# Kernel tuning notes

Hardware: AMD Instinct MI355X
Metric: run time of the kernel (lower is better)

Reference implementation:

```python
import jax, jax.numpy as jnp
import numpy as np
from jax import lax

B = 8192          # batched independent VAD frames (original module is batch=1 streaming)
CUTOFF = 129      # STFT_CUTOFF
STRIDE = 128      # STFT_STRIDE
NFFT = 256        # STFT kernel length (inferred: pad 576->640, stride 128 -> 4 frames)
H = 128           # LSTM hidden size


def conv1d(x, w, b=None, stride=1, padding=0):
    # x: [B, Cin, T], w: [Cout, Cin, K]
    y = lax.conv_general_dilated(x, w, (stride,), [(padding, padding)],
                                 dimension_numbers=("NCH", "OIH", "NCH"))
    if b is not None:
        y = y + b[None, :, None]
    return y


def setup_inputs() -> dict:
    key = jax.random.key(0)
    ks = jax.random.split(key, 40)
    f32 = jnp.float32

    def rn(i, shape, scale=0.1):
        return jax.random.normal(ks[i], shape, dtype=f32) * scale

    inp = {
        "audio": jax.random.normal(ks[0], (B, 576), dtype=f32),
        "h": jnp.zeros((B, H), dtype=f32),
        "c": jnp.zeros((B, H), dtype=f32),
        # STFT basis: 129 real + 129 imag cosine/sine rows, kernel 256
        "forward_basis": rn(1, (2 * CUTOFF, 1, NFFT), 0.1),
        # encoder: 4 conv1d+relu blocks (Silero v5 layout)
        "enc_w1": rn(2, (128, 129, 3)), "enc_b1": rn(3, (128,)),
        "enc_w2": rn(4, (64, 128, 3)), "enc_b2": rn(5, (64,)),
        "enc_w3": rn(6, (64, 64, 3)),  "enc_b3": rn(7, (64,)),
        "enc_w4": rn(8, (128, 64, 3)), "enc_b4": rn(9, (128,)),
        # LSTM cell weights
        "wi": rn(10, (H, H)), "wf": rn(11, (H, H)), "wg": rn(12, (H, H)), "wo": rn(13, (H, H)),
        "ui": rn(14, (H, H)), "uf": rn(15, (H, H)), "ug": rn(16, (H, H)), "uo": rn(17, (H, H)),
        "bxi": rn(18, (H,)), "bxf": rn(19, (H,)), "bxg": rn(20, (H,)), "bxo": rn(21, (H,)),
        "bhi": rn(22, (H,)), "bhf": rn(23, (H,)), "bhg": rn(24, (H,)), "bho": rn(25, (H,)),
        # output head: conv1d 128 -> 1, kernel 1
        "conv_w": rn(26, (1, H, 1)), "conv_b": rn(27, (1,)),
    }
    return inp


def reference(audio, h, c, forward_basis,
              enc_w1, enc_b1, enc_w2, enc_b2, enc_w3, enc_b3, enc_w4, enc_b4,
              wi, wf, wg, wo, ui, uf, ug, uo,
              bxi, bxf, bxg, bxo, bhi, bhf, bhg, bho,
              conv_w, conv_b):
    # STFT via strided conv1d on reflect-padded audio
    x = jnp.pad(audio, ((0, 0), (0, 64)), mode="reflect")[:, None, :]   # [B,1,640]
    x = conv1d(x, forward_basis, stride=STRIDE)                          # [B,258,4]
    real, imag = x[:, :CUTOFF, :], x[:, CUTOFF:, :]
    mag = jnp.sqrt(real ** 2 + imag ** 2)                                # [B,129,4]

    # encoder: conv+relu stack, T: 4 -> 4 -> 2 -> 1 -> 1
    e = jax.nn.relu(conv1d(mag, enc_w1, enc_b1, stride=1, padding=1))
    e = jax.nn.relu(conv1d(e, enc_w2, enc_b2, stride=2, padding=1))
    e = jax.nn.relu(conv1d(e, enc_w3, enc_b3, stride=2, padding=1))
    e = jax.nn.relu(conv1d(e, enc_w4, enc_b4, stride=1, padding=1))
    x = e[:, :, 0]                                                       # [B,128]

    lin = lambda v, W, b: v @ W.T + b
    i_gate = jax.nn.sigmoid(lin(x, wi, bxi) + lin(h, ui, bhi))
    f_gate = jax.nn.sigmoid(lin(x, wf, bxf) + lin(h, uf, bhf))
    g_gate = jnp.tanh(lin(x, wg, bxg) + lin(h, ug, bhg))
    o_gate = jax.nn.sigmoid(lin(x, wo, bxo) + lin(h, uo, bho))
    c_out = f_gate * c + i_gate * g_gate
    h_out = o_gate * jnp.tanh(c_out)

    # output head: relu -> conv1d(128->1, k=1) -> sigmoid -> mean over T(=1)
    y = jax.nn.relu(h_out)                                               # [B,128]
    logit = y @ conv_w[0, :, 0] + conv_b[0]                              # [B]
    prob = jax.nn.sigmoid(logit)[:, None]                                # [B,1]
    return prob, h_out, c_out
```

## Files before the change

kernel.cpp:

```cpp
#include <hip/hip_runtime.h>
#include <math.h>

#define BATCH 8192
typedef unsigned short u16;
typedef unsigned int u32;
typedef __attribute__((ext_vector_type(8))) short bf16x8;
typedef __attribute__((ext_vector_type(4))) float f32x4;
typedef __attribute__((ext_vector_type(4))) unsigned short u16x4;

__device__ __forceinline__ float sigm(float v) { return 1.0f / (1.0f + __expf(-v)); }
__device__ __forceinline__ u16 f2bf(float f) {
    union { float f; u32 u; } v; v.f = f;
    u32 r = v.u + 0x7FFFu + ((v.u >> 16) & 1u);
    return (u16)(r >> 16);
}
__device__ __forceinline__ float bf2f(u16 h) {
    union { u32 u; float f; } v; v.u = ((u32)h) << 16; return v.f;
}
__device__ __forceinline__ void split_store4(float4 v, u16* hp, u16* lp) {
    u16 h0 = f2bf(v.x), h1 = f2bf(v.y), h2 = f2bf(v.z), h3 = f2bf(v.w);
    u16x4 hv = {h0, h1, h2, h3};
    u16x4 lv = {f2bf(v.x - bf2f(h0)), f2bf(v.y - bf2f(h1)),
                f2bf(v.z - bf2f(h2)), f2bf(v.w - bf2f(h3))};
    *(u16x4*)hp = hv; *(u16x4*)lp = lv;
}
__device__ __forceinline__ bf16x8 bfrag(const u16* Bf, int nt, int ch, int nch, int lane) {
    return *(const bf16x8*)(Bf + (((size_t)nt * nch + ch) * 64 + lane) * 8);
}
#define MFMA(a, b, c) __builtin_amdgcn_mfma_f32_16x16x32_bf16(a, b, c, 0, 0, 0)

#define S_FBT 69632
#define S_B1  61440
#define S_B2A 16384
#define S_B2B 24576
#define S_B3  8192
#define S_B4  8192
#define S_BL  131072
#define P_FBT 0
#define P_B1  139264
#define P_B2A 262144
#define P_B2B 294912
#define P_B3  344064
#define P_B4  360448
#define P_BL  376832
#define WEND  638976
#define N_PREP 319488

__global__ __launch_bounds__(256) void k_prep(const float* __restrict__ fb,
                                              const float* __restrict__ w1, const float* __restrict__ w2,
                                              const float* __restrict__ w3, const float* __restrict__ w4,
                                              const float* __restrict__ wi, const float* __restrict__ wf,
                                              const float* __restrict__ wg, const float* __restrict__ wo,
                                              const float* __restrict__ ui, const float* __restrict__ uf,
                                              const float* __restrict__ ug, const float* __restrict__ uo,
                                              u16* __restrict__ wsu) {
    const float* Ws[8] = {wi, wf, wg, wo, ui, uf, ug, uo};
    for (int i = blockIdx.x * 256 + threadIdx.x; i < N_PREP; i += gridDim.x * 256) {
        int r = i;
        float v; int P, S, idx;
        if (r < S_FBT) {
            int f = r >> 9, lane = (r & 511) >> 3, e = r & 7;
            int n = (f >> 3) * 16 + (lane & 15), k = (f & 7) * 32 + (lane >> 4) * 8 + e;
            int c = n >> 1, part = n & 1;
            v = (n < 258) ? fb[(size_t)(c + part * 129) * 256 + k] : 0.f;
            P = P_FBT; S = S_FBT; idx = r;
        } else if ((r -= S_FBT) < S_B1) {
            int kk = r / 20480, r2 = r - kk * 20480;
            int f = r2 >> 9, lane = (r2 & 511) >> 3, e = r2 & 7;
            int n = (f / 5) * 16 + (lane & 15), k = (f % 5) * 32 + (lane >> 4) * 8 + e;
            v = (k < 129) ? w1[(size_t)n * 387 + k * 3 + kk] : 0.f;
            P = P_B1; S = S_B1; idx = r;
        } else if ((r -= S_B1) < S_B2A) {
            int f = r >> 9, lane = (r & 511) >> 3, e = r & 7;
            int n = (f >> 3) * 16 + (lane & 15), k = (f & 7) * 32 + (lane >> 4) * 8 + e;
            v = w2[(size_t)n * 384 + (k & 127) * 3 + (k >> 7) + 1];
            P = P_B2A; S = S_B2A; idx = r;
        } else if ((r -= S_B2A) < S_B2B) {
            int f = r >> 9, lane = (r & 511) >> 3, e = r & 7;
            int n = (f / 12) * 16 + (lane & 15), k = (f % 12) * 32 + (lane >> 4) * 8 + e;
            v = w2[(size_t)n * 384 + (k & 127) * 3 + (k >> 7)];
            P = P_B2B; S = S_B2B; idx = r;
        } else if ((r -= S_B2B) < S_B3) {
            int f = r >> 9, lane = (r & 511) >> 3, e = r & 7;
            int n = (f >> 2) * 16 + (lane & 15), k = (f & 3) * 32 + (lane >> 4) * 8 + e;
            v = w3[(size_t)n * 192 + (k & 63) * 3 + (k >> 6) + 1];
            P = P_B3; S = S_B3; idx = r;
        } else if ((r -= S_B3) < S_B4) {
            int f = r >> 9, lane = (r & 511) >> 3, e = r & 7;
            int n = (f >> 1) * 16 + (lane & 15), k = (f & 1) * 32 + (lane >> 4) * 8 + e;
            v = w4[(size_t)n * 192 + k * 3 + 1];
            P = P_B4; S = S_B4; idx = r;
        } else {
            r -= S_B4;
            int f = r >> 9, lane = (r & 511) >> 3, e = r & 7;
            int n = (f >> 3) * 16 + (lane & 15), k = (f & 7) * 32 + (lane >> 4) * 8 + e;
            int g = n >> 7, j = n & 127;
            v = Ws[g + ((k >= 128) ? 4 : 0)][(size_t)j * 128 + (k & 127)];
            P = P_BL; S = S_BL; idx = r;
        }
        u16 h = f2bf(v);
        wsu[P + idx] = h;
        wsu[P + S + idx] = f2bf(v - bf2f(h));
    }
}

__global__ __launch_bounds__(512) void k_fused1(const float* __restrict__ audio,
                                                const u16* __restrict__ wsu,
                                                const float* __restrict__ b1,
                                                float* __restrict__ act) {
    __shared__ __align__(16) u16 aAh[8 * 680];
    __shared__ __align__(16) u16 aAl[8 * 680];
    __shared__ __align__(16) u16 mAh[8 * 6 * 168];
    __shared__ __align__(16) u16 mAl[8 * 6 * 168];
    const int tid = threadIdx.x;
    const int b0 = blockIdx.x << 3;
    for (int i = tid; i < 4032; i += 512) {
        ((u32*)mAh)[i] = 0u;
        ((u32*)mAl)[i] = 0u;
    }
    for (int i = tid; i < 8 * 160; i += 512) {
        int bb = i / 160, j4 = (i - bb * 160) * 4;
        const float* ap = audio + (size_t)(b0 + bb) * 576;
        float4 v;
        if (j4 < 576) v = *(const float4*)(ap + j4);
        else { v.x = ap[1150 - j4]; v.y = ap[1149 - j4]; v.z = ap[1148 - j4]; v.w = ap[1147 - j4]; }
        int phys = bb * 680 + j4 + (j4 >> 7) * 8;
        split_store4(v, aAh + phys, aAl + phys);
    }
    __syncthreads();
    const int lane = tid & 63, w = tid >> 6;
    const int m = lane & 15, quad = lane >> 4;
    const u16* fbT = wsu + P_FBT;
    const int tcnt = (w == 7) ? 3 : 2;
    f32x4 acc[2][3];
    #pragma unroll
    for (int mt = 0; mt < 2; ++mt)
        #pragma unroll
        for (int t = 0; t < 3; ++t) acc[mt][t] = (f32x4){0.f, 0.f, 0.f, 0.f};
    for (int ch = 0; ch < 8; ++ch) {
        bf16x8 ah[2], al[2];
        #pragma unroll
        for (int mt = 0; mt < 2; ++mt) {
            int Rm = mt * 16 + m;
            int phys = (Rm >> 2) * 680 + (Rm & 3) * 136 + ch * 32 + quad * 8 + ((ch >= 4) ? 8 : 0);
            ah[mt] = *(const bf16x8*)(aAh + phys);
            al[mt] = *(const bf16x8*)(aAl + phys);
        }
        #pragma unroll
        for (int tt = 0; tt < 3; ++tt) {
            if (tt < tcnt) {
                int t = w * 2 + tt;
                bf16x8 bh = bfrag(fbT, t, ch, 8, lane);
                bf16x8 bl_ = bfrag(fbT + S_FBT, t, ch, 8, lane);
                #pragma unroll
                for (int mt = 0; mt < 2; ++mt) {
                    acc[mt][tt] = MFMA(ah[mt], bh, acc[mt][tt]);
                    acc[mt][tt] = MFMA(ah[mt], bl_, acc[mt][tt]);
                    acc[mt][tt] = MFMA(al[mt], bh, acc[mt][tt]);
                }
            }
        }
    }
    #pragma unroll
    for (int tt = 0; tt < 3; ++tt) {
        if (tt < tcnt) {
            int n = (w * 2 + tt) * 16 + m;
            #pragma unroll
            for (int mt = 0; mt < 2; ++mt)
                #pragma unroll
                for (int r = 0; r < 4; ++r) {
                    float vv = acc[mt][tt][r];
                    float s = vv * vv;
                    s += __shfl_xor(s, 1);
                    if (!(n & 1)) {
                        int R = mt * 16 + quad * 4 + r;
                        int bb = R >> 2, t = R & 3, c = n >> 1;
                        float sv = sqrtf(s);
                        u16 h = f2bf(sv);
                        int phys = (bb * 6 + t + 1) * 168 + c;
                        mAh[phys] = h;
                        mAl[phys] = f2bf(sv - bf2f(h));
                    }
                }
        }
    }
    __syncthreads();
    const u16* B1h = wsu + P_B1;
    const u16* B1l = wsu + P_B1 + S_B1;
    f32x4 acc2[2];
    acc2[0] = (f32x4){0.f, 0.f, 0.f, 0.f};
    acc2[1] = (f32x4){0.f, 0.f, 0.f, 0.f};
    for (int kk = 0; kk < 3; ++kk) {
        for (int ch = 0; ch < 5; ++ch) {
            bf16x8 bh = bfrag(B1h + kk * 20480, w, ch, 5, lane);
            bf16x8 bl_ = bfrag(B1l + kk * 20480, w, ch, 5, lane);
            #pragma unroll
            for (int mt = 0; mt < 2; ++mt) {
                int Rm = mt * 16 + m;
                int phys = ((Rm >> 2) * 6 + (Rm & 3) + kk) * 168 + ch * 32 + quad * 8;
                bf16x8 ah = *(const bf16x8*)(mAh + phys);
                bf16x8 al = *(const bf16x8*)(mAl + phys);
                acc2[mt] = MFMA(ah, bh, acc2[mt]);
                acc2[mt] = MFMA(ah, bl_, acc2[mt]);
                acc2[mt] = MFMA(al, bh, acc2[mt]);
            }
        }
    }
    {
        int n = w * 16 + m;
        float bv = b1[n];
        #pragma unroll
        for (int mt = 0; mt < 2; ++mt)
            #pragma unroll
            for (int r = 0; r < 4; ++r) {
                int R = mt * 16 + quad * 4 + r;
                act[(size_t)(b0 + (R >> 2)) * 512 + (R & 3) * 128 + n] = fmaxf(acc2[mt][r] + bv, 0.f);
            }
    }
}

__global__ __launch_bounds__(512) void k_fused2(const float* __restrict__ act,
                                                const float* __restrict__ hin,
                                                const u16* __restrict__ wsu,
                                                const float* __restrict__ cin,
                                                const float* __restrict__ b2, const float* __restrict__ b3,
                                                const float* __restrict__ b4,
                                                const float* __restrict__ bxi, const float* __restrict__ bxf,
                                                const float* __restrict__ bxg, const float* __restrict__ bxo,
                                                const float* __restrict__ bhi, const float* __restrict__ bhf,
                                                const float* __restrict__ bhg, const float* __restrict__ bho,
                                                const float* __restrict__ cw, const float* __restrict__ cb,
                                                float* __restrict__ out) {
    __shared__ __align__(16) u16 eAh[16 * 520];
    __shared__ __align__(16) u16 eAl[16 * 520];
    __shared__ __align__(16) u16 s2h[16 * 136];
    __shared__ __align__(16) u16 s2l[16 * 136];
    __shared__ __align__(16) u16 s3h[16 * 72];
    __shared__ __align__(16) u16 s3l[16 * 72];
    __shared__ __align__(16) u16 xhh[16 * 264];
    __shared__ __align__(16) u16 xhl[16 * 264];
    __shared__ float pr[8][16];
    const int tid = threadIdx.x;
    const int b0 = blockIdx.x << 4;
    for (int i = tid; i < 16 * 128; i += 512) {
        int row = i >> 7, c4 = (i & 127) * 4;
        float4 v = *(const float4*)(act + (size_t)(b0 + row) * 512 + c4);
        split_store4(v, eAh + row * 520 + c4, eAl + row * 520 + c4);
    }
    for (int i = tid; i < 16 * 32; i += 512) {
        int row = i >> 5, c4 = (i & 31) * 4;
        float4 v = *(const float4*)(hin + (size_t)(b0 + row) * 128 + c4);
        split_store4(v, xhh + row * 264 + 128 + c4, xhl + row * 264 + 128 + c4);
    }
    __syncthreads();
    const int lane = tid & 63, w = tid >> 6;
    const int m = lane & 15, quad = lane >> 4;
    {
        const int isB = w >> 2, nt = w & 3;
        const int awoff = isB ? 128 : 0;
        const int nch = isB ? 12 : 8;
        const u16* Bh = wsu + (isB ? P_B2B : P_B2A);
        const u16* Bl = Bh + (isB ? S_B2B : S_B2A);
        f32x4 acc = (f32x4){0.f, 0.f, 0.f, 0.f};
        for (int ch = 0; ch < nch; ++ch) {
            int phys = m * 520 + awoff + ch * 32 + quad * 8;
            bf16x8 ah = *(const bf16x8*)(eAh + phys);
            bf16x8 al = *(const bf16x8*)(eAl + phys);
            bf16x8 bh = bfrag(Bh, nt, ch, nch, lane);
            bf16x8 bl_ = bfrag(Bl, nt, ch, nch, lane);
            acc = MFMA(ah, bh, acc);
            acc = MFMA(ah, bl_, acc);
            acc = MFMA(al, bh, acc);
        }
        const int oc = nt * 16 + m;
        const float bv = b2[oc];
        const int col = isB * 64 + oc;
        #pragma unroll
        for (int r = 0; r < 4; ++r) {
            int row = quad * 4 + r;
            float vv = fmaxf(acc[r] + bv, 0.f);
            u16 h = f2bf(vv);
            s2h[row * 136 + col] = h;
            s2l[row * 136 + col] = f2bf(vv - bf2f(h));
        }
    }
    __syncthreads();
    if (w < 4) {
        const u16* Bh = wsu + P_B3;
        const u16* Bl = Bh + S_B3;
        f32x4 acc = (f32x4){0.f, 0.f, 0.f, 0.f};
        for (int ch = 0; ch < 4; ++ch) {
            int phys = m * 136 + ch * 32 + quad * 8;
            bf16x8 ah = *(const bf16x8*)(s2h + phys);
            bf16x8 al = *(const bf16x8*)(s2l + phys);
            bf16x8 bh = bfrag(Bh, w, ch, 4, lane);
            bf16x8 bl_ = bfrag(Bl, w, ch, 4, lane);
            acc = MFMA(ah, bh, acc);
            acc = MFMA(ah, bl_, acc);
            acc = MFMA(al, bh, acc);
        }
        const int n = w * 16 + m;
        const float bv = b3[n];
        #pragma unroll
        for (int r = 0; r < 4; ++r) {
            int row = quad * 4 + r;
            float vv = fmaxf(acc[r] + bv, 0.f);
            u16 h = f2bf(vv);
            s3h[row * 72 + n] = h;
            s3l[row * 72 + n] = f2bf(vv - bf2f(h));
        }
    }
    __syncthreads();
    {
        const u16* Bh = wsu + P_B4;
        const u16* Bl = Bh + S_B4;
        f32x4 acc = (f32x4){0.f, 0.f, 0.f, 0.f};
        for (int ch = 0; ch < 2; ++ch) {
            int phys = m * 72 + ch * 32 + quad * 8;
            bf16x8 ah = *(const bf16x8*)(s3h + phys);
            bf16x8 al = *(const bf16x8*)(s3l + phys);
            bf16x8 bh = bfrag(Bh, w, ch, 2, lane);
            bf16x8 bl_ = bfrag(Bl, w, ch, 2, lane);
            acc = MFMA(ah, bh, acc);
            acc = MFMA(ah, bl_, acc);
            acc = MFMA(al, bh, acc);
        }
        const int n = w * 16 + m;
        const float bv = b4[n];
        #pragma unroll
        for (int r = 0; r < 4; ++r) {
            int row = quad * 4 + r;
            float vv = fmaxf(acc[r] + bv, 0.f);
            u16 h = f2bf(vv);
            xhh[row * 264 + n] = h;
            xhl[row * 264 + n] = f2bf(vv - bf2f(h));
        }
    }
    __syncthreads();
    {
        const u16* BLh = wsu + P_BL;
        const u16* BLl = BLh + S_BL;
        f32x4 acc[4];
        #pragma unroll
        for (int g = 0; g < 4; ++g) acc[g] = (f32x4){0.f, 0.f, 0.f, 0.f};
        for (int ch = 0; ch < 8; ++ch) {
            int phys = m * 264 + ch * 32 + quad * 8;
            bf16x8 ah = *(const bf16x8*)(xhh + phys);
            bf16x8 al = *(const bf16x8*)(xhl + phys);
            #pragma unroll
            for (int g = 0; g < 4; ++g) {
                int nt = g * 8 + w;
                bf16x8 bh = bfrag(BLh, nt, ch, 8, lane);
                bf16x8 bl_ = bfrag(BLl, nt, ch, 8, lane);
                acc[g] = MFMA(ah, bh, acc[g]);
                acc[g] = MFMA(ah, bl_, acc[g]);
                acc[g] = MFMA(al, bh, acc[g]);
            }
        }
        float partial[4];
        const int j = w * 16 + m;
        const float bi = bxi[j] + bhi[j];
        const float bff = bxf[j] + bhf[j];
        const float bgg = bxg[j] + bhg[j];
        const float boo = bxo[j] + bho[j];
        const float cwj = cw[j];
        #pragma unroll
        for (int r = 0; r < 4; ++r) {
            const int b = b0 + quad * 4 + r;
            const float ig = sigm(acc[0][r] + bi);
            const float fg = sigm(acc[1][r] + bff);
            const float gg = tanhf(acc[2][r] + bgg);
            const float og = sigm(acc[3][r] + boo);
            const float ci = cin[(size_t)b * 128 + j];
            const float co = fg * ci + ig * gg;
            const float ho = og * tanhf(co);
            out[(size_t)BATCH + (size_t)b * 128 + j] = ho;
            out[(size_t)BATCH + (size_t)BATCH * 128 + (size_t)b * 128 + j] = co;
            partial[r] = fmaxf(ho, 0.f) * cwj;
        }
        #pragma unroll
        for (int off = 1; off < 16; off <<= 1)
            #pragma unroll
            for (int r = 0; r < 4; ++r) partial[r] += __shfl_xor(partial[r], off);
        if (m == 0) {
            #pragma unroll
            for (int r = 0; r < 4; ++r) pr[w][quad * 4 + r] = partial[r];
        }
    }
    __syncthreads();
    if (tid < 16) {
        float s = cb[0];
        #pragma unroll
        for (int g = 0; g < 8; ++g) s += pr[g][tid];
        out[b0 + tid] = sigm(s);
    }
}

extern "C" void kernel_launch(void* const* d_in, const int* in_sizes, int n_in,
                              void* d_out, int out_size, void* d_ws, size_t ws_size,
                              hipStream_t stream) {
    const float* audio = (const float*)d_in[0];
    const float* hin   = (const float*)d_in[1];
    const float* cin   = (const float*)d_in[2];
    const float* fb    = (const float*)d_in[3];
    const float* w1    = (const float*)d_in[4];
    const float* b1    = (const float*)d_in[5];
    const float* w2    = (const float*)d_in[6];
    const float* b2    = (const float*)d_in[7];
    const float* w3    = (const float*)d_in[8];
    const float* b3    = (const float*)d_in[9];
    const float* w4    = (const float*)d_in[10];
    const float* b4    = (const float*)d_in[11];
    const float* wi    = (const float*)d_in[12];
    const float* wf    = (const float*)d_in[13];
    const float* wg    = (const float*)d_in[14];
    const float* wo    = (const float*)d_in[15];
    const float* ui    = (const float*)d_in[16];
    const float* uf    = (const float*)d_in[17];
    const float* ug    = (const float*)d_in[18];
    const float* uo    = (const float*)d_in[19];
    const float* bxi   = (const float*)d_in[20];
    const float* bxf   = (const float*)d_in[21];
    const float* bxg   = (const float*)d_in[22];
    const float* bxo   = (const float*)d_in[23];
    const float* bhi   = (const float*)d_in[24];
    const float* bhf   = (const float*)d_in[25];
    const float* bhg   = (const float*)d_in[26];
    const float* bho   = (const float*)d_in[27];
    const float* cw    = (const float*)d_in[28];
    const float* cb    = (const float*)d_in[29];
    float* out = (float*)d_out;

    u16* wsu = (u16*)d_ws;
    float* ACT = (float*)(wsu + WEND);

    k_prep<<<640, 256, 0, stream>>>(fb, w1, w2, w3, w4, wi, wf, wg, wo, ui, uf, ug, uo, wsu);
    k_fused1<<<BATCH / 8, 512, 0, stream>>>(audio, wsu, b1, ACT);
    k_fused2<<<BATCH / 16, 512, 0, stream>>>(ACT, hin, wsu, cin, b2, b3, b4,
                                             bxi, bxf, bxg, bxo, bhi, bhf, bhg, bho,
                                             cw, cb, out);
}
```

Before: 188.0 us.

## Double batch tile in k_fused1, alias shared buffers, pass bf16 hi/lo split

k_fused1 now processes 16 frames per block instead of 8, so each B-fragment of the STFT and conv1 weights is reused across four M-tiles. The audio and magnitude shared buffers are aliased into one union, which needs an extra barrier and a re-zero pass between the phases. The intermediate activation is written as precomputed bf16 hi/lo halves instead of fp32, so k_fused2 only copies them and no longer does the split. In exchange, register pressure rises from the larger accumulator arrays and the grid has half as many blocks.

```diff
diff --git a/kernel.cpp b/kernel.cpp
--- a/kernel.cpp
+++ b/kernel.cpp
@@ -107,24 +107,21 @@
 __global__ __launch_bounds__(512) void k_fused1(const float* __restrict__ audio,
                                                 const u16* __restrict__ wsu,
                                                 const float* __restrict__ b1,
-                                                float* __restrict__ act) {
-    __shared__ __align__(16) u16 aAh[8 * 680];
-    __shared__ __align__(16) u16 aAl[8 * 680];
-    __shared__ __align__(16) u16 mAh[8 * 6 * 168];
-    __shared__ __align__(16) u16 mAl[8 * 6 * 168];
+                                                u16* __restrict__ E1H, u16* __restrict__ E1L) {
+    __shared__ __align__(16) u16 uni[32256];
+    u16* aAh = uni;
+    u16* aAl = uni + 11520;
+    u16* mAh = uni;
+    u16* mAl = uni + 16128;
     const int tid = threadIdx.x;
-    const int b0 = blockIdx.x << 3;
-    for (int i = tid; i < 4032; i += 512) {
-        ((u32*)mAh)[i] = 0u;
-        ((u32*)mAl)[i] = 0u;
-    }
-    for (int i = tid; i < 8 * 160; i += 512) {
+    const int b0 = blockIdx.x << 4;
+    for (int i = tid; i < 16 * 160; i += 512) {
         int bb = i / 160, j4 = (i - bb * 160) * 4;
         const float* ap = audio + (size_t)(b0 + bb) * 576;
         float4 v;
         if (j4 < 576) v = *(const float4*)(ap + j4);
         else { v.x = ap[1150 - j4]; v.y = ap[1149 - j4]; v.z = ap[1148 - j4]; v.w = ap[1147 - j4]; }
-        int phys = bb * 680 + j4 + (j4 >> 7) * 8;
+        int phys = bb * 720 + j4 + (j4 >> 7) * 8;
         split_store4(v, aAh + phys, aAl + phys);
     }
     __syncthreads();
@@ -132,17 +129,17 @@
     const int m = lane & 15, quad = lane >> 4;
     const u16* fbT = wsu + P_FBT;
     const int tcnt = (w == 7) ? 3 : 2;
-    f32x4 acc[2][3];
+    f32x4 acc[4][3];
     #pragma unroll
-    for (int mt = 0; mt < 2; ++mt)
+    for (int mt = 0; mt < 4; ++mt)
         #pragma unroll
         for (int t = 0; t < 3; ++t) acc[mt][t] = (f32x4){0.f, 0.f, 0.f, 0.f};
     for (int ch = 0; ch < 8; ++ch) {
-        bf16x8 ah[2], al[2];
-        #pragma unroll
-        for (int mt = 0; mt < 2; ++mt) {
+        bf16x8 ah[4], al[4];
+        #pragma unroll
+        for (int mt = 0; mt < 4; ++mt) {
             int Rm = mt * 16 + m;
-            int phys = (Rm >> 2) * 680 + (Rm & 3) * 136 + ch * 32 + quad * 8 + ((ch >= 4) ? 8 : 0);
+            int phys = (Rm >> 2) * 720 + (Rm & 3) * 136 + ch * 32 + quad * 8 + ((ch >= 4) ? 8 : 0);
             ah[mt] = *(const bf16x8*)(aAh + phys);
             al[mt] = *(const bf16x8*)(aAl + phys);
         }
@@ -153,7 +150,7 @@
                 bf16x8 bh = bfrag(fbT, t, ch, 8, lane);
                 bf16x8 bl_ = bfrag(fbT + S_FBT, t, ch, 8, lane);
                 #pragma unroll
-                for (int mt = 0; mt < 2; ++mt) {
+                for (int mt = 0; mt < 4; ++mt) {
                     acc[mt][tt] = MFMA(ah[mt], bh, acc[mt][tt]);
                     acc[mt][tt] = MFMA(ah[mt], bl_, acc[mt][tt]);
                     acc[mt][tt] = MFMA(al[mt], bh, acc[mt][tt]);
@@ -161,12 +158,15 @@
             }
         }
     }
+    __syncthreads();
+    for (int i = tid; i < 16128; i += 512) ((u32*)uni)[i] = 0u;
+    __syncthreads();
     #pragma unroll
     for (int tt = 0; tt < 3; ++tt) {
         if (tt < tcnt) {
             int n = (w * 2 + tt) * 16 + m;
             #pragma unroll
-            for (int mt = 0; mt < 2; ++mt)
+            for (int mt = 0; mt < 4; ++mt)
                 #pragma unroll
                 for (int r = 0; r < 4; ++r) {
                     float vv = acc[mt][tt][r];
@@ -187,15 +187,15 @@
     __syncthreads();
     const u16* B1h = wsu + P_B1;
     const u16* B1l = wsu + P_B1 + S_B1;
-    f32x4 acc2[2];
-    acc2[0] = (f32x4){0.f, 0.f, 0.f, 0.f};
-    acc2[1] = (f32x4){0.f, 0.f, 0.f, 0.f};
+    f32x4 acc2[4];
+    #pragma unroll
+    for (int mt = 0; mt < 4; ++mt) acc2[mt] = (f32x4){0.f, 0.f, 0.f, 0.f};
     for (int kk = 0; kk < 3; ++kk) {
         for (int ch = 0; ch < 5; ++ch) {
             bf16x8 bh = bfrag(B1h + kk * 20480, w, ch, 5, lane);
             bf16x8 bl_ = bfrag(B1l + kk * 20480, w, ch, 5, lane);
             #pragma unroll
-            for (int mt = 0; mt < 2; ++mt) {
+            for (int mt = 0; mt < 4; ++mt) {
                 int Rm = mt * 16 + m;
                 int phys = ((Rm >> 2) * 6 + (Rm & 3) + kk) * 168 + ch * 32 + quad * 8;
                 bf16x8 ah = *(const bf16x8*)(mAh + phys);
@@ -210,16 +210,20 @@
         int n = w * 16 + m;
         float bv = b1[n];
         #pragma unroll
-        for (int mt = 0; mt < 2; ++mt)
+        for (int mt = 0; mt < 4; ++mt)
             #pragma unroll
             for (int r = 0; r < 4; ++r) {
                 int R = mt * 16 + quad * 4 + r;
-                act[(size_t)(b0 + (R >> 2)) * 512 + (R & 3) * 128 + n] = fmaxf(acc2[mt][r] + bv, 0.f);
+                float vv = fmaxf(acc2[mt][r] + bv, 0.f);
+                u16 h = f2bf(vv);
+                size_t idx = (size_t)(b0 + (R >> 2)) * 512 + (R & 3) * 128 + n;
+                E1H[idx] = h;
+                E1L[idx] = f2bf(vv - bf2f(h));
             }
     }
 }
 
-__global__ __launch_bounds__(512) void k_fused2(const float* __restrict__ act,
+__global__ __launch_bounds__(512) void k_fused2(const u16* __restrict__ E1H, const u16* __restrict__ E1L,
                                                 const float* __restrict__ hin,
                                                 const u16* __restrict__ wsu,
                                                 const float* __restrict__ cin,
@@ -242,10 +246,10 @@
     __shared__ float pr[8][16];
     const int tid = threadIdx.x;
     const int b0 = blockIdx.x << 4;
-    for (int i = tid; i < 16 * 128; i += 512) {
-        int row = i >> 7, c4 = (i & 127) * 4;
-        float4 v = *(const float4*)(act + (size_t)(b0 + row) * 512 + c4);
-        split_store4(v, eAh + row * 520 + c4, eAl + row * 520 + c4);
+    for (int i = tid; i < 16 * 64; i += 512) {
+        int row = i >> 6, c8 = (i & 63) * 8;
+        *(uint4*)(eAh + row * 520 + c8) = *(const uint4*)(E1H + (size_t)(b0 + row) * 512 + c8);
+        *(uint4*)(eAl + row * 520 + c8) = *(const uint4*)(E1L + (size_t)(b0 + row) * 512 + c8);
     }
     for (int i = tid; i < 16 * 32; i += 512) {
         int row = i >> 5, c4 = (i & 31) * 4;
@@ -432,11 +436,12 @@
     float* out = (float*)d_out;
 
     u16* wsu = (u16*)d_ws;
-    float* ACT = (float*)(wsu + WEND);
+    u16* E1H = wsu + WEND;
+    u16* E1L = E1H + (size_t)BATCH * 512;
 
     k_prep<<<640, 256, 0, stream>>>(fb, w1, w2, w3, w4, wi, wf, wg, wo, ui, uf, ug, uo, wsu);
-    k_fused1<<<BATCH / 8, 512, 0, stream>>>(audio, wsu, b1, ACT);
-    k_fused2<<<BATCH / 16, 512, 0, stream>>>(ACT, hin, wsu, cin, b2, b3, b4,
+    k_fused1<<<BATCH / 16, 512, 0, stream>>>(audio, wsu, b1, E1H, E1L);
+    k_fused2<<<BATCH / 16, 512, 0, stream>>>(E1H, E1L, hin, wsu, cin, b2, b3, b4,
                                              bxi, bxf, bxg, bxo, bhi, bhf, bhg, bho,
                                              cw, cb, out);
 }
```

Result: faster. 181.4 us (-3.5%).
